# Kernel optimization log

Measured on AMD Instinct MI355X. Metric: run time of the kernel, lower is better.

## Reference

```python
import jax, jax.numpy as jnp
import numpy as np

TEMPERATURE = 0.07
BRANCH, DEPTH = 16, 3   # balanced tree: 4096 leaves, 4368 non-root nodes, max_dep K = 3
N1, DPROJ = 1024, 1024
EPS = 1e-6


def _build_tree(b, D):
    """Replicates Tree(): balanced tree, leaves = ids 0..b^D-1, internal nodes after, root last."""
    L = b ** D
    offsets, off = {}, 0
    for d in range(D, 0, -1):          # depth D (leaves) .. depth 1
        offsets[d] = off
        off += b ** d
    M = off                             # number of non-root nodes (= len(tree.father))
    root = M
    father = np.empty(M, np.int64)
    for d in range(D, 0, -1):
        ids = offsets[d] + np.arange(b ** d)
        father[ids] = root if d == 1 else offsets[d - 1] + np.arange(b ** d) // b
    # subtree[n] = descendants of n incl. self (bool over non-root node ids)
    S = np.zeros((M, M), bool)
    S[np.arange(M), np.arange(M)] = True
    for d in range(D, 1, -1):
        ids = offsets[d] + np.arange(b ** d)
        agg = S[ids].reshape(b ** (d - 1), b, M).any(1)
        par = offsets[d - 1] + np.arange(b ** (d - 1))
        S[par] |= agg
    # ancestor of each leaf at every depth
    anc = {D: np.arange(L)}
    for d in range(D - 1, 0, -1):
        anc[d] = father[anc[d + 1]]
    K = D
    pos = np.zeros((K, L, M), bool)
    neg = np.zeros((K, L, M), bool)
    msk = np.zeros((K, L), bool)
    for d in range(D, 0, -1):           # node depth d -> mask slot d-1 (gen_leaf_item)
        nd = d - 1
        nodes = anc[d]
        msk[nd] = True
        pos[nd] = S[nodes] if d == D else (S[nodes] ^ S[anc[d + 1]])
        neg[nd] = ~S[nodes]
    depth = np.full(L, float(D), np.float32)
    return pos, neg, msk, depth, M, L


def setup_inputs() -> dict:
    pos, neg, msk, depth, M, L = _build_tree(BRANCH, DEPTH)
    key = jax.random.key(0)
    kq, kv, kl = jax.random.split(key, 3)
    q = jax.random.normal(kq, (N1, DPROJ), jnp.float32)
    vitual_center = jax.random.normal(kv, (M, DPROJ), jnp.float32)
    labels = jax.random.randint(kl, (N1,), 0, L)
    return {
        "q": q,
        "vitual_center": vitual_center,
        "labels": labels,
        "pos_down2up": jnp.asarray(pos),
        "neg_down2up": jnp.asarray(neg),
        "mask": jnp.asarray(msk),
        "depth": jnp.asarray(depth),
    }


def _forward(q, vitual_center, labels, pos_down2up, neg_down2up, mask, depth):
    K = pos_down2up.shape[0]           # = max_dep
    M = vitual_center.shape[0]
    n1 = q.shape[0]
    # k = all_gather(q).detach() on one device, then concat virtual centers
    k = jnp.concatenate([jax.lax.stop_gradient(q), vitual_center], axis=0)   # [N2, d]
    k_labels = jnp.concatenate([labels, jnp.arange(M)], axis=0)              # [N2]
    # cosine similarity (F.normalize clamps norm at 1e-12)
    qn = q / jnp.maximum(jnp.linalg.norm(q, axis=-1, keepdims=True), 1e-12)
    kn = k / jnp.maximum(jnp.linalg.norm(k, axis=-1, keepdims=True), 1e-12)
    logits = (qn @ kn.T) / TEMPERATURE                                       # [N1, N2]
    # gen_label_mask: relation[:, q_labels, k_labels] -> [K, N1, N2]
    pm = pos_down2up[:, labels][:, :, k_labels].astype(logits.dtype)
    nm = neg_down2up[:, labels][:, :, k_labels].astype(logits.dtype)
    l3 = logits[None]                                                        # [1, N1, N2]
    pos_logits = jnp.sum(l3 * pm, -1) / jnp.maximum(jnp.sum(pm, -1), EPS)    # [K, N1]
    full = jnp.concatenate([pos_logits[..., None], l3 * nm], axis=-1)        # [K, N1, N2+1]
    # cross_entropy with target class 0, reduction='none'
    ce = jax.nn.logsumexp(full, axis=-1) - full[..., 0]                      # [K, N1]
    now_depth = depth[labels][None, :]                                       # [K, N1] via broadcast
    now_mask = mask[:, labels].astype(ce.dtype)                              # [K, N1]
    loss = jnp.sum(ce / now_depth * now_mask) / n1 * K
    return loss


def reference(q, vitual_center, labels, pos_down2up, neg_down2up, mask, depth):
    loss = _forward(q, vitual_center, labels, pos_down2up, neg_down2up, mask, depth)
    return (loss, loss)
```

## Files before the change

kernel.cpp:

```cpp
#include <hip/hip_runtime.h>
#include <math.h>

#define N1 1024
#define DPROJ 1024
#define M_NODES 4368
#define N2 (N1 + M_NODES)
#define N2P 5504
#define L_LEAVES 4096
#define INV_T (1.0f / 0.07f)
#define NBX 43

typedef __bf16 bf16;
typedef __bf16 bf16x4v __attribute__((ext_vector_type(4)));
typedef __bf16 bf16x8 __attribute__((ext_vector_type(8)));
typedef float f32x4 __attribute__((ext_vector_type(4)));

__global__ __launch_bounds__(256) void normalize_kernel(
    const float* __restrict__ q, const float* __restrict__ vc,
    bf16* __restrict__ kn, float* __restrict__ out) {
  const int row = blockIdx.x;
  if (row == 0 && threadIdx.x == 0) { out[0] = 0.f; out[1] = 0.f; }
  bf16x4v* dst = (bf16x4v*)(kn + (size_t)row * DPROJ);
  if (row >= N2) {
    bf16x4v z = {(bf16)0.f, (bf16)0.f, (bf16)0.f, (bf16)0.f};
    dst[threadIdx.x] = z;
    return;
  }
  const float* src = (row < N1) ? q + (size_t)row * DPROJ
                                : vc + (size_t)(row - N1) * DPROJ;
  float4 v = ((const float4*)src)[threadIdx.x];
  float s = v.x * v.x + v.y * v.y + v.z * v.z + v.w * v.w;
  for (int off = 32; off > 0; off >>= 1) s += __shfl_down(s, off);
  __shared__ float wsum[4];
  const int lane = threadIdx.x & 63, wid = threadIdx.x >> 6;
  if (lane == 0) wsum[wid] = s;
  __syncthreads();
  const float tot = wsum[0] + wsum[1] + wsum[2] + wsum[3];
  const float inv = 1.0f / fmaxf(sqrtf(tot), 1e-12f);
  bf16x4v o = {(bf16)(v.x * inv), (bf16)(v.y * inv), (bf16)(v.z * inv),
               (bf16)(v.w * inv)};
  dst[threadIdx.x] = o;
}

#define BM 64
#define BN 128
#define BK 64
#define NT (DPROJ / BK)

__device__ __forceinline__ void gload16(const bf16* g, bf16* l) {
  __builtin_amdgcn_global_load_lds(
      (const __attribute__((address_space(1))) void*)g,
      (__attribute__((address_space(3))) void*)l, 16, 0, 0);
}

__global__ __launch_bounds__(256, 3) void gemm_loss_kernel(
    const bf16* __restrict__ kn, const int* __restrict__ labels,
    float* __restrict__ partials) {
  __shared__ bf16 As[2][BM][BK];
  __shared__ bf16 Bs[2][BN][BK];
  __shared__ int lab_r[BM];
  __shared__ int lab_c[BN];
  __shared__ float blk_part[BM][2][6];
  const int wg = blockIdx.y * NBX + blockIdx.x;
  const int vid = (wg & 7) * 86 + (wg >> 3);
  const int bx = vid >> 4;
  const int by = vid & 15;
  const int j0 = bx * BN;
  const int i0 = by * BM;
  const int t = threadIdx.x;
  const int lane = t & 63, w = t >> 6;
  const int wm = w >> 1, wn = w & 1;

  if (t < BM) lab_r[t] = labels[i0 + t];
  if (t < BN && j0 + t < N1) lab_c[t] = labels[j0 + t];

  f32x4 acc[2][4] = {};

  const int rik = lane >> 3;
  const int kswz = ((lane & 7) ^ ((lane >> 3) & 7)) * 8;
  const bf16* gA0 = kn + (size_t)(i0 + w * 16 + rik) * DPROJ + kswz;
  const bf16* gA1 = gA0 + (size_t)8 * DPROJ;
  const bf16* gB0 = kn + (size_t)(j0 + w * 32 + rik) * DPROJ + kswz;
  const bf16* gB1 = gB0 + (size_t)8 * DPROJ;
  const bf16* gB2 = gB0 + (size_t)16 * DPROJ;
  const bf16* gB3 = gB0 + (size_t)24 * DPROJ;

  const int ar = wm * 32 + (lane & 15);
  const int br = wn * 64 + (lane & 15);
  const int l7 = lane & 7;
  const int g4 = lane >> 4;
  const int kf0 = ((g4 ^ l7)) * 8;
  const int kf1 = (((4 + g4) ^ l7)) * 8;

#define STAGE(buf, k0)                             \
  do {                                             \
    gload16(gA0 + (k0), &As[buf][w * 16][0]);      \
    gload16(gA1 + (k0), &As[buf][w * 16 + 8][0]);  \
    gload16(gB0 + (k0), &Bs[buf][w * 32][0]);      \
    gload16(gB1 + (k0), &Bs[buf][w * 32 + 8][0]);  \
    gload16(gB2 + (k0), &Bs[buf][w * 32 + 16][0]); \
    gload16(gB3 + (k0), &Bs[buf][w * 32 + 24][0]); \
  } while (0)

  STAGE(0, 0);
  __syncthreads();

#pragma unroll 2
  for (int it = 0; it < NT; ++it) {
    const int cur = it & 1;
    if (it + 1 < NT) {
      STAGE(cur ^ 1, (it + 1) * BK);
      asm volatile("s_waitcnt vmcnt(6)" ::: "memory");
    } else {
      asm volatile("s_waitcnt vmcnt(0)" ::: "memory");
    }
    __builtin_amdgcn_s_barrier();

    bf16x8 a0[2], a1[2], b0[4], b1[4];
#pragma unroll
    for (int m = 0; m < 2; ++m) {
      a0[m] = *(const bf16x8*)&As[cur][ar + m * 16][kf0];
      a1[m] = *(const bf16x8*)&As[cur][ar + m * 16][kf1];
    }
#pragma unroll
    for (int n = 0; n < 4; ++n) {
      b0[n] = *(const bf16x8*)&Bs[cur][br + n * 16][kf0];
      b1[n] = *(const bf16x8*)&Bs[cur][br + n * 16][kf1];
    }
#pragma unroll
    for (int m = 0; m < 2; ++m)
#pragma unroll
      for (int n = 0; n < 4; ++n) {
        acc[m][n] = __builtin_amdgcn_mfma_f32_16x16x32_bf16(
            a0[m], b0[n], acc[m][n], 0, 0, 0);
        acc[m][n] = __builtin_amdgcn_mfma_f32_16x16x32_bf16(
            a1[m], b1[n], acc[m][n], 0, 0, 0);
      }

    __builtin_amdgcn_s_barrier();
  }

  const int g = lane >> 4;
  const int p = lane & 15;
#pragma unroll
  for (int m = 0; m < 2; ++m) {
#pragma unroll
    for (int j = 0; j < 4; ++j) {
      const int rloc = wm * 32 + m * 16 + g * 4 + j;
      const int lab = lab_r[rloc];
      const int a2 = lab >> 4, a1 = lab >> 8;
      float ps0 = 0, ps1 = 0, ps2 = 0, ns0 = 0, ns1 = 0, ns2 = 0;
#pragma unroll
      for (int n = 0; n < 4; ++n) {
        const int cloc = wn * 64 + n * 16 + p;
        const int gc = j0 + cloc;
        if (gc < N2) {
          const int nid = (gc < N1) ? lab_c[cloc] : (gc - N1);
          const bool isLeaf = nid < L_LEAVES;
          const bool isD2 = (nid >= L_LEAVES) && (nid < L_LEAVES + 256);
          const bool eq = (nid == lab);
          const bool inS2 =
              (nid == L_LEAVES + a2) || (isLeaf && ((nid >> 4) == a2));
          const bool inS1 = (nid == L_LEAVES + 256 + a1) ||
                            (isD2 && (((nid - L_LEAVES) >> 4) == a1)) ||
                            (isLeaf && ((nid >> 8) == a1));
          const float v = acc[m][n][j] * INV_T;
          const float e = __expf(v);
          if (eq) ps2 += v; else ns2 += e;
          if (inS2) { if (!eq) ps1 += v; } else ns1 += e;
          if (inS1) { if (!inS2) ps0 += v; } else ns0 += e;
        }
      }
#pragma unroll
      for (int msk = 1; msk < 16; msk <<= 1) {
        ps0 += __shfl_xor(ps0, msk);
        ps1 += __shfl_xor(ps1, msk);
        ps2 += __shfl_xor(ps2, msk);
        ns0 += __shfl_xor(ns0, msk);
        ns1 += __shfl_xor(ns1, msk);
        ns2 += __shfl_xor(ns2, msk);
      }
      if (p == 0) {
        float* d = &blk_part[rloc][wn][0];
        d[0] = ps0; d[1] = ps1; d[2] = ps2;
        d[3] = ns0; d[4] = ns1; d[5] = ns2;
      }
    }
  }
  __syncthreads();
  for (int idx = t; idx < BM * 6; idx += 256) {
    const int r = idx / 6, k = idx % 6;
    const float val = blk_part[r][0][k] + blk_part[r][1][k];
    partials[((size_t)(i0 + r) * NBX + bx) * 6 + k] = val;
  }
}

__global__ __launch_bounds__(256) void finalize_kernel(
    const float* __restrict__ partials, const int* __restrict__ labels,
    const float* __restrict__ depth, float* __restrict__ out) {
  __shared__ int hist_s[M_NODES];
  const int t = threadIdx.x;
  for (int i = t; i < M_NODES; i += 256) hist_s[i] = 0;
  __syncthreads();
  for (int i = t; i < N1; i += 256) {
    const int lb = labels[i];
    atomicAdd(&hist_s[lb], 1);
    atomicAdd(&hist_s[L_LEAVES + (lb >> 4)], 1);
    atomicAdd(&hist_s[L_LEAVES + 256 + (lb >> 8)], 1);
  }
  __syncthreads();

  const int row = blockIdx.x * 256 + t;
  const int lab = labels[row];
  const int a2 = lab >> 4, a1 = lab >> 8;
  const int cEq = hist_s[lab] + 1;
  const int cS2 = hist_s[L_LEAVES + a2] + 17;
  const int cS1 = hist_s[L_LEAVES + 256 + a1] + 273;
  float ps0 = 0, ps1 = 0, ps2 = 0, ns0 = 0, ns1 = 0, ns2 = 0;
  const float* pp = partials + (size_t)row * NBX * 6;
  for (int b = 0; b < NBX; ++b) {
    ps0 += pp[b * 6 + 0];
    ps1 += pp[b * 6 + 1];
    ps2 += pp[b * 6 + 2];
    ns0 += pp[b * 6 + 3];
    ns1 += pp[b * 6 + 4];
    ns2 += pp[b * 6 + 5];
  }
  float ce = 0.f;
  {
    float pl = ps2 / fmaxf((float)cEq, 1e-6f);
    ce += logf(ns2 + (float)cEq + __expf(pl)) - pl;
  }
  {
    float pl = ps1 / fmaxf((float)(cS2 - cEq), 1e-6f);
    ce += logf(ns1 + (float)cS2 + __expf(pl)) - pl;
  }
  {
    float pl = ps0 / fmaxf((float)(cS1 - cS2), 1e-6f);
    ce += logf(ns0 + (float)cS1 + __expf(pl)) - pl;
  }
  float contrib = ce / depth[lab] * (3.0f / (float)N1);
  for (int off = 32; off > 0; off >>= 1) contrib += __shfl_down(contrib, off);
  __shared__ float wsum[4];
  const int lane = t & 63, wid = t >> 6;
  if (lane == 0) wsum[wid] = contrib;
  __syncthreads();
  if (t == 0) {
    const float tot = wsum[0] + wsum[1] + wsum[2] + wsum[3];
    atomicAdd(&out[0], tot);
    atomicAdd(&out[1], tot);
  }
}

extern "C" void kernel_launch(void* const* d_in, const int* in_sizes, int n_in,
                              void* d_out, int out_size, void* d_ws,
                              size_t ws_size, hipStream_t stream) {
  const float* q = (const float*)d_in[0];
  const float* vc = (const float*)d_in[1];
  const int* labels = (const int*)d_in[2];
  const float* depth = (const float*)d_in[6];
  float* out = (float*)d_out;

  bf16* kn = (bf16*)d_ws;
  float* partials = (float*)((char*)d_ws + (size_t)N2P * DPROJ * sizeof(bf16));

  normalize_kernel<<<N2P, 256, 0, stream>>>(q, vc, kn, out);

  dim3 grid(NBX, N1 / BM);
  gemm_loss_kernel<<<grid, 256, 0, stream>>>(kn, labels, partials);

  finalize_kernel<<<4, 256, 0, stream>>>(partials, labels, depth, out);
}
```

Measured before the change: 48.82 us.

## Switch normalized embeddings and GEMM from bf16 to fp8 MFMA

The normalize kernel now writes unit-norm rows as packed fp8 instead of bf16. The similarity GEMM loads 8-byte fp8 fragments and uses the fp8 16x16x32 MFMA. This halves global, LDS and workspace traffic and lets occupancy rise to 5 waves per EU. The cost is much coarser logits: the values are scaled by 1/0.07 before logsumexp, so fp8 rounding may push the loss outside tolerance. The LDS swizzle and staging layout were reworked to match the byte-sized elements.

```diff
diff --git a/kernel.cpp b/kernel.cpp
--- a/kernel.cpp
+++ b/kernel.cpp
@@ -10,20 +10,16 @@
 #define INV_T (1.0f / 0.07f)
 #define NBX 43
 
-typedef __bf16 bf16;
-typedef __bf16 bf16x4v __attribute__((ext_vector_type(4)));
-typedef __bf16 bf16x8 __attribute__((ext_vector_type(8)));
 typedef float f32x4 __attribute__((ext_vector_type(4)));
 
 __global__ __launch_bounds__(256) void normalize_kernel(
     const float* __restrict__ q, const float* __restrict__ vc,
-    bf16* __restrict__ kn, float* __restrict__ out) {
+    unsigned char* __restrict__ kn, float* __restrict__ out) {
   const int row = blockIdx.x;
   if (row == 0 && threadIdx.x == 0) { out[0] = 0.f; out[1] = 0.f; }
-  bf16x4v* dst = (bf16x4v*)(kn + (size_t)row * DPROJ);
+  int* dst = (int*)(kn + (size_t)row * DPROJ);
   if (row >= N2) {
-    bf16x4v z = {(bf16)0.f, (bf16)0.f, (bf16)0.f, (bf16)0.f};
-    dst[threadIdx.x] = z;
+    dst[threadIdx.x] = 0;
     return;
   }
   const float* src = (row < N1) ? q + (size_t)row * DPROJ
@@ -37,9 +33,9 @@
   __syncthreads();
   const float tot = wsum[0] + wsum[1] + wsum[2] + wsum[3];
   const float inv = 1.0f / fmaxf(sqrtf(tot), 1e-12f);
-  bf16x4v o = {(bf16)(v.x * inv), (bf16)(v.y * inv), (bf16)(v.z * inv),
-               (bf16)(v.w * inv)};
-  dst[threadIdx.x] = o;
+  int p = __builtin_amdgcn_cvt_pk_fp8_f32(v.x * inv, v.y * inv, 0, false);
+  p = __builtin_amdgcn_cvt_pk_fp8_f32(v.z * inv, v.w * inv, p, true);
+  dst[threadIdx.x] = p;
 }
 
 #define BM 64
@@ -47,17 +43,18 @@
 #define BK 64
 #define NT (DPROJ / BK)
 
-__device__ __forceinline__ void gload16(const bf16* g, bf16* l) {
+__device__ __forceinline__ void gload16(const unsigned char* g,
+                                        unsigned char* l) {
   __builtin_amdgcn_global_load_lds(
       (const __attribute__((address_space(1))) void*)g,
       (__attribute__((address_space(3))) void*)l, 16, 0, 0);
 }
 
-__global__ __launch_bounds__(256, 3) void gemm_loss_kernel(
-    const bf16* __restrict__ kn, const int* __restrict__ labels,
+__global__ __launch_bounds__(256, 5) void gemm_loss_kernel(
+    const unsigned char* __restrict__ kn, const int* __restrict__ labels,
     float* __restrict__ partials) {
-  __shared__ bf16 As[2][BM][BK];
-  __shared__ bf16 Bs[2][BN][BK];
+  __shared__ unsigned char As[2][BM][BK];
+  __shared__ unsigned char Bs[2][BN][BK];
   __shared__ int lab_r[BM];
   __shared__ int lab_c[BN];
   __shared__ float blk_part[BM][2][6];
@@ -76,30 +73,24 @@
 
   f32x4 acc[2][4] = {};
 
-  const int rik = lane >> 3;
-  const int kswz = ((lane & 7) ^ ((lane >> 3) & 7)) * 8;
-  const bf16* gA0 = kn + (size_t)(i0 + w * 16 + rik) * DPROJ + kswz;
-  const bf16* gA1 = gA0 + (size_t)8 * DPROJ;
-  const bf16* gB0 = kn + (size_t)(j0 + w * 32 + rik) * DPROJ + kswz;
-  const bf16* gB1 = gB0 + (size_t)8 * DPROJ;
-  const bf16* gB2 = gB0 + (size_t)16 * DPROJ;
-  const bf16* gB3 = gB0 + (size_t)24 * DPROJ;
+  const int rik = lane >> 2;
+  const int gswz = ((lane & 3) ^ ((lane >> 3) & 3)) * 16;
+  const unsigned char* gA = kn + (size_t)(i0 + w * 16 + rik) * DPROJ + gswz;
+  const unsigned char* gB0 = kn + (size_t)(j0 + w * 16 + rik) * DPROJ + gswz;
+  const unsigned char* gB1 = gB0 + (size_t)64 * DPROJ;
 
   const int ar = wm * 32 + (lane & 15);
   const int br = wn * 64 + (lane & 15);
-  const int l7 = lane & 7;
+  const int x2 = 2 * ((lane >> 1) & 3);
   const int g4 = lane >> 4;
-  const int kf0 = ((g4 ^ l7)) * 8;
-  const int kf1 = (((4 + g4) ^ l7)) * 8;
-
-#define STAGE(buf, k0)                             \
-  do {                                             \
-    gload16(gA0 + (k0), &As[buf][w * 16][0]);      \
-    gload16(gA1 + (k0), &As[buf][w * 16 + 8][0]);  \
-    gload16(gB0 + (k0), &Bs[buf][w * 32][0]);      \
-    gload16(gB1 + (k0), &Bs[buf][w * 32 + 8][0]);  \
-    gload16(gB2 + (k0), &Bs[buf][w * 32 + 16][0]); \
-    gload16(gB3 + (k0), &Bs[buf][w * 32 + 24][0]); \
+  const int kf0 = (g4 ^ x2) * 8;
+  const int kf1 = ((4 + g4) ^ x2) * 8;
+
+#define STAGE(buf, k0)                            \
+  do {                                            \
+    gload16(gA + (k0), &As[buf][w * 16][0]);      \
+    gload16(gB0 + (k0), &Bs[buf][w * 16][0]);     \
+    gload16(gB1 + (k0), &Bs[buf][w * 16 + 64][0]);\
   } while (0)
 
   STAGE(0, 0);
@@ -110,30 +101,30 @@
     const int cur = it & 1;
     if (it + 1 < NT) {
       STAGE(cur ^ 1, (it + 1) * BK);
-      asm volatile("s_waitcnt vmcnt(6)" ::: "memory");
+      asm volatile("s_waitcnt vmcnt(3)" ::: "memory");
     } else {
       asm volatile("s_waitcnt vmcnt(0)" ::: "memory");
     }
     __builtin_amdgcn_s_barrier();
 
-    bf16x8 a0[2], a1[2], b0[4], b1[4];
+    long a0[2], a1[2], b0[4], b1[4];
 #pragma unroll
     for (int m = 0; m < 2; ++m) {
-      a0[m] = *(const bf16x8*)&As[cur][ar + m * 16][kf0];
-      a1[m] = *(const bf16x8*)&As[cur][ar + m * 16][kf1];
+      a0[m] = *(const long*)&As[cur][ar + m * 16][kf0];
+      a1[m] = *(const long*)&As[cur][ar + m * 16][kf1];
     }
 #pragma unroll
     for (int n = 0; n < 4; ++n) {
-      b0[n] = *(const bf16x8*)&Bs[cur][br + n * 16][kf0];
-      b1[n] = *(const bf16x8*)&Bs[cur][br + n * 16][kf1];
+      b0[n] = *(const long*)&Bs[cur][br + n * 16][kf0];
+      b1[n] = *(const long*)&Bs[cur][br + n * 16][kf1];
     }
 #pragma unroll
     for (int m = 0; m < 2; ++m)
 #pragma unroll
       for (int n = 0; n < 4; ++n) {
-        acc[m][n] = __builtin_amdgcn_mfma_f32_16x16x32_bf16(
+        acc[m][n] = __builtin_amdgcn_mfma_f32_16x16x32_fp8_fp8(
             a0[m], b0[n], acc[m][n], 0, 0, 0);
-        acc[m][n] = __builtin_amdgcn_mfma_f32_16x16x32_bf16(
+        acc[m][n] = __builtin_amdgcn_mfma_f32_16x16x32_fp8_fp8(
             a1[m], b1[n], acc[m][n], 0, 0, 0);
       }
 
@@ -261,8 +252,8 @@
   const float* depth = (const float*)d_in[6];
   float* out = (float*)d_out;
 
-  bf16* kn = (bf16*)d_ws;
-  float* partials = (float*)((char*)d_ws + (size_t)N2P * DPROJ * sizeof(bf16));
+  unsigned char* kn = (unsigned char*)d_ws;
+  float* partials = (float*)((char*)d_ws + (size_t)N2P * DPROJ);
 
   normalize_kernel<<<N2P, 256, 0, stream>>>(q, vc, kn, out);
 
```

After: 45.69 us. 1.07x faster.
